# Kernel tuning notes

Hardware: AMD Instinct MI355X
Metric: run time of the kernel (lower is better)

Reference implementation:

```python
import jax, jax.numpy as jnp
import numpy as np

BITS_W = 2  # WAGE default weight bitwidth


def _scale(bits):
    return 2.0 ** (bits - 1)


def quantize_w(x):
    """WAGE Quantize.W: clip to [-1+delta, 1-delta], round to grid of step delta,
    with straight-through estimator for gradients."""
    s = _scale(BITS_W)
    delta = 1.0 / s
    xc = jnp.clip(x, -1.0 + delta, 1.0 - delta)
    y = jnp.round(xc * s) / s
    # straight-through: forward uses y, gradient flows as identity to x
    return x + jax.lax.stop_gradient(y - x)


def setup_inputs() -> dict:
    key = jax.random.key(0)
    k1, k2 = jax.random.split(key)
    B, D_IN, C_OUT = 16384, 1024, 1024
    inputs = jax.random.normal(k1, (B, D_IN), dtype=jnp.float32)
    # learned kernel per build(): shape [d_in, c_out]
    kernel = jax.random.normal(k2, (D_IN, C_OUT), dtype=jnp.float32) * 0.5
    return {"inputs": inputs, "kernel": kernel}


def reference(inputs, kernel):
    # quantize weights every forward pass, then dense matmul
    return jnp.matmul(inputs, quantize_w(kernel))
```

## Files before the change

kernel.cpp:

```cpp
#include <hip/hip_runtime.h>

typedef unsigned short u16;
typedef unsigned int u32;

typedef __bf16 bf16x8 __attribute__((ext_vector_type(8)));
typedef float floatx4 __attribute__((ext_vector_type(4)));


__device__ __forceinline__ u32 f2bf(float f) {
    u32 u = __builtin_bit_cast(u32, f);
    return (u + 0x7fffu + ((u >> 16) & 1u)) >> 16;
}

__device__ __forceinline__ float quant_w(float x) {
    float xc = fminf(fmaxf(x, -0.5f), 0.5f);
    return rintf(xc * 2.0f) * 0.5f;
}

__device__ __forceinline__ void gload_lds16(const u16* g, u16* l) {
    __builtin_amdgcn_global_load_lds(
        (const __attribute__((address_space(1))) void*)g,
        (__attribute__((address_space(3))) void*)l,
        16, 0, 0);
}


__global__ __launch_bounds__(256) void cast_a_kernel(const float4* __restrict__ in,
                                                     uint4* __restrict__ out) {
    int t = blockIdx.x * 256 + threadIdx.x;
    float4 a = in[2 * t];
    float4 b = in[2 * t + 1];
    uint4 o;
    o.x = f2bf(a.x) | (f2bf(a.y) << 16);
    o.y = f2bf(a.z) | (f2bf(a.w) << 16);
    o.z = f2bf(b.x) | (f2bf(b.y) << 16);
    o.w = f2bf(b.z) | (f2bf(b.w) << 16);
    out[t] = o;
}


__global__ __launch_bounds__(256) void quant_transpose_kernel(const float* __restrict__ W,
                                                              u16* __restrict__ Bt) {
    __shared__ u16 tile[32][33];
    const int KN = 1024;
    int tx = threadIdx.x;
    int ty = threadIdx.y;
    int k0 = blockIdx.y * 32;
    int n0 = blockIdx.x * 32;
#pragma unroll
    for (int i = 0; i < 4; i++) {
        int kl = ty + i * 8;
        float x = W[(k0 + kl) * KN + n0 + tx];
        tile[kl][tx] = (u16)f2bf(quant_w(x));
    }
    __syncthreads();
#pragma unroll
    for (int i = 0; i < 4; i++) {
        int nl = ty + i * 8;
        Bt[(n0 + nl) * KN + k0 + tx] = tile[tx][nl];
    }
}


__global__ __launch_bounds__(512, 2) void gemm_4region_kernel(const u16* __restrict__ A,
                                                              const u16* __restrict__ Bt,
                                                              float* __restrict__ C) {
    const int K = 1024;
    const int N = 1024;

    __shared__ alignas(16) u16 As[2 * 2 * 128 * 64];
    __shared__ alignas(16) u16 Bs[2 * 2 * 128 * 64];

    const int tid = threadIdx.x;
    const int lane = tid & 63;
    const int wid = tid >> 6;
    const int wm = wid >> 2;
    const int wn = wid & 3;
    const int frow = lane & 15;
    const int fkc = lane >> 4;
    const int rsw = frow & 7;
    const int mbase = blockIdx.x * 256;
    const int nbase = blockIdx.y * 256;

    const int sr = tid >> 3;
    const int gc = (tid & 7) ^ (sr & 7);

    const u16* Abase = &A[(size_t)(mbase + sr) * K + gc * 8];
    const u16* Bbase = &Bt[(size_t)(nbase + sr) * K + gc * 8];

    floatx4 acc[8][4] = {};
    bf16x8 af0[4][2], af1[4][2], bf0[2][2], bf1[2][2];

    auto stage = [&](int tau, int q) {
        const int hf = q & 1;
        const int isA = q >> 1;
        const u16* gb = isA ? Abase : Bbase;
        u16* lb = isA ? As : Bs;
        const size_t goff = (size_t)(hf * 128) * K + (size_t)tau * 64;
        u16* dst = &lb[(((tau & 1) * 2 + hf) * 8192) + tid * 8];
        gload_lds16(gb + goff, dst);
        gload_lds16(gb + goff + (size_t)64 * K, dst + 4096);
    };

#define LGKM0() asm volatile("s_waitcnt lgkmcnt(0)" ::: "memory")
#define VMC(n)  asm volatile("s_waitcnt vmcnt(" #n ")" ::: "memory")
#define BAR()                          \
    __builtin_amdgcn_sched_barrier(0); \
    __builtin_amdgcn_s_barrier();      \
    __builtin_amdgcn_sched_barrier(0)

#define READ_AF0(b)                                                                  \
    _Pragma("unroll") for (int mf = 0; mf < 4; mf++)                                 \
        _Pragma("unroll") for (int s = 0; s < 2; s++)                                \
            af0[mf][s] = *(const bf16x8*)&As[(((b)*2 + wm) * 128 + mf * 16 + frow) * 64 + \
                                             (((s * 4 + fkc) ^ rsw) * 8)]
#define READ_AF1(b)                                                                  \
    _Pragma("unroll") for (int mf = 0; mf < 4; mf++)                                 \
        _Pragma("unroll") for (int s = 0; s < 2; s++)                                \
            af1[mf][s] = *(const bf16x8*)&As[(((b)*2 + wm) * 128 + 64 + mf * 16 + frow) * 64 + \
                                             (((s * 4 + fkc) ^ rsw) * 8)]
#define READ_BF0(b)                                                                  \
    _Pragma("unroll") for (int nf = 0; nf < 2; nf++)                                 \
        _Pragma("unroll") for (int s = 0; s < 2; s++)                                \
            bf0[nf][s] = *(const bf16x8*)&Bs[(((b)*2 + (wn >> 1)) * 128 + (wn & 1) * 64 + nf * 16 + frow) * 64 + \
                                             (((s * 4 + fkc) ^ rsw) * 8)]
#define READ_BF1(b)                                                                  \
    _Pragma("unroll") for (int nf = 0; nf < 2; nf++)                                 \
        _Pragma("unroll") for (int s = 0; s < 2; s++)                                \
            bf1[nf][s] = *(const bf16x8*)&Bs[(((b)*2 + (wn >> 1)) * 128 + (wn & 1) * 64 + 32 + nf * 16 + frow) * 64 + \
                                             (((s * 4 + fkc) ^ rsw) * 8)]
#define MFMA_CL(af, bf, mo, no)                                                      \
    __builtin_amdgcn_s_setprio(1);                                                   \
    _Pragma("unroll") for (int mf = 0; mf < 4; mf++)                                 \
        _Pragma("unroll") for (int nf = 0; nf < 2; nf++)                             \
            _Pragma("unroll") for (int s = 0; s < 2; s++)                            \
                acc[(mo) + mf][(no) + nf] = __builtin_amdgcn_mfma_f32_16x16x32_bf16( \
                    af[mf][s], bf[nf][s], acc[(mo) + mf][(no) + nf], 0, 0, 0);       \
    __builtin_amdgcn_s_setprio(0)

    stage(0, 0); stage(0, 1); stage(0, 2); stage(0, 3);
    stage(1, 0); stage(1, 1); stage(1, 2); stage(1, 3);
    VMC(8);
    BAR();

    for (int t = 0; t < 16; t++) {
        const int b = t & 1;

        if (t > 0) { MFMA_CL(af1, bf1, 4, 2); }
        READ_AF0(b);
        READ_BF0(b);
        LGKM0();
        BAR();

        MFMA_CL(af0, bf0, 0, 0);
        READ_AF1(b);
        LGKM0();
        BAR();

        MFMA_CL(af1, bf0, 4, 0);
        READ_BF1(b);
        if (t <= 13) { stage(t + 2, 2); stage(t + 2, 3); }
        LGKM0();
        BAR();

        MFMA_CL(af0, bf1, 0, 2);
        if (t <= 13) {
            stage(t + 2, 0); stage(t + 2, 1);
            VMC(8);
        } else if (t == 14) {
            VMC(0);
        }
        BAR();
    }

    MFMA_CL(af1, bf1, 4, 2);

#undef LGKM0
#undef VMC
#undef BAR
#undef READ_AF0
#undef READ_AF1
#undef READ_BF0
#undef READ_BF1
#undef MFMA_CL

    const int crow = (lane >> 4) * 4;
    const int ccol = lane & 15;
#pragma unroll
    for (int i = 0; i < 8; i++) {
#pragma unroll
        for (int j = 0; j < 4; j++) {
            float* cp = &C[(size_t)(mbase + wm * 128 + i * 16 + crow) * N +
                           nbase + wn * 64 + j * 16 + ccol];
#pragma unroll
            for (int r = 0; r < 4; r++) cp[r * N] = acc[i][j][r];
        }
    }
}


extern "C" void kernel_launch(void* const* d_in, const int* in_sizes, int n_in,
                              void* d_out, int out_size, void* d_ws, size_t ws_size,
                              hipStream_t stream) {
    const float* A = (const float*)d_in[0];
    const float* W = (const float*)d_in[1];
    float* C = (float*)d_out;

    u16* Abf = (u16*)d_ws;
    u16* Btq = (u16*)((char*)d_ws + (size_t)33554432);

    cast_a_kernel<<<8192, 256, 0, stream>>>((const float4*)A, (uint4*)Abf);
    quant_transpose_kernel<<<dim3(32, 32), dim3(32, 8), 0, stream>>>(W, Btq);
    gemm_4region_kernel<<<dim3(64, 4), 512, 0, stream>>>(Abf, Btq, C);
}
```

Before: 145.2 us.

## Restructure GEMM main loop into two barrier regions with split-row staging

The GEMM main loop drops from four barrier-separated regions per K-step to two. Each tile's global-to-LDS loads are split into two row halves: one half is issued two steps ahead and the other one step ahead, with matching vmcnt waits. All A and B fragment reads are now issued together before three back-to-back MFMA clusters, cutting barrier count and sync stalls at the cost of more live registers and tighter load/compute overlap. The cast kernel also has each thread convert two chunks, halving its grid size.

```diff
diff --git a/kernel.cpp b/kernel.cpp
--- a/kernel.cpp
+++ b/kernel.cpp
@@ -28,14 +28,17 @@
 __global__ __launch_bounds__(256) void cast_a_kernel(const float4* __restrict__ in,
                                                      uint4* __restrict__ out) {
     int t = blockIdx.x * 256 + threadIdx.x;
-    float4 a = in[2 * t];
-    float4 b = in[2 * t + 1];
-    uint4 o;
-    o.x = f2bf(a.x) | (f2bf(a.y) << 16);
-    o.y = f2bf(a.z) | (f2bf(a.w) << 16);
-    o.z = f2bf(b.x) | (f2bf(b.y) << 16);
-    o.w = f2bf(b.z) | (f2bf(b.w) << 16);
-    out[t] = o;
+#pragma unroll
+    for (int u = 0; u < 2; u++) {
+        float4 a = in[4 * t + 2 * u];
+        float4 b = in[4 * t + 2 * u + 1];
+        uint4 o;
+        o.x = f2bf(a.x) | (f2bf(a.y) << 16);
+        o.y = f2bf(a.z) | (f2bf(a.w) << 16);
+        o.z = f2bf(b.x) | (f2bf(b.y) << 16);
+        o.w = f2bf(b.z) | (f2bf(b.w) << 16);
+        out[2 * t + u] = o;
+    }
 }
 
 
@@ -62,7 +65,7 @@
 }
 
 
-__global__ __launch_bounds__(512, 2) void gemm_4region_kernel(const u16* __restrict__ A,
+__global__ __launch_bounds__(512, 2) void gemm_2region_kernel(const u16* __restrict__ A,
                                                               const u16* __restrict__ Bt,
                                                               float* __restrict__ C) {
     const int K = 1024;
@@ -84,22 +87,28 @@
 
     const int sr = tid >> 3;
     const int gc = (tid & 7) ^ (sr & 7);
-
-    const u16* Abase = &A[(size_t)(mbase + sr) * K + gc * 8];
-    const u16* Bbase = &Bt[(size_t)(nbase + sr) * K + gc * 8];
+    const int brow0 = ((sr >> 5) << 6) | (sr & 31);
 
     floatx4 acc[8][4] = {};
     bf16x8 af0[4][2], af1[4][2], bf0[2][2], bf1[2][2];
 
-    auto stage = [&](int tau, int q) {
-        const int hf = q & 1;
-        const int isA = q >> 1;
-        const u16* gb = isA ? Abase : Bbase;
-        u16* lb = isA ? As : Bs;
-        const size_t goff = (size_t)(hf * 128) * K + (size_t)tau * 64;
-        u16* dst = &lb[(((tau & 1) * 2 + hf) * 8192) + tid * 8];
-        gload_lds16(gb + goff, dst);
-        gload_lds16(gb + goff + (size_t)64 * K, dst + 4096);
+    auto astage = [&](int tau, int u) {
+        const int row = sr + u * 64;
+#pragma unroll
+        for (int hf = 0; hf < 2; hf++) {
+            const u16* g = &A[(size_t)(mbase + hf * 128 + row) * K + (size_t)tau * 64 + gc * 8];
+            u16* dst = &As[(((tau & 1) * 2 + hf) * 8192) + row * 64 + (tid & 7) * 8];
+            gload_lds16(g, dst);
+        }
+    };
+    auto bstage = [&](int tau, int u) {
+        const int row = brow0 + u * 32;
+#pragma unroll
+        for (int hf = 0; hf < 2; hf++) {
+            const u16* g = &Bt[(size_t)(nbase + hf * 128 + row) * K + (size_t)tau * 64 + gc * 8];
+            u16* dst = &Bs[(((tau & 1) * 2 + hf) * 8192) + row * 64 + (tid & 7) * 8];
+            gload_lds16(g, dst);
+        }
     };
 
 #define LGKM0() asm volatile("s_waitcnt lgkmcnt(0)" ::: "memory")
@@ -138,8 +147,9 @@
                     af[mf][s], bf[nf][s], acc[(mo) + mf][(no) + nf], 0, 0, 0);       \
     __builtin_amdgcn_s_setprio(0)
 
-    stage(0, 0); stage(0, 1); stage(0, 2); stage(0, 3);
-    stage(1, 0); stage(1, 1); stage(1, 2); stage(1, 3);
+    astage(0, 0); bstage(0, 0);
+    astage(0, 1); bstage(0, 1);
+    astage(1, 0); bstage(1, 0);
     VMC(8);
     BAR();
 
@@ -149,27 +159,27 @@
         if (t > 0) { MFMA_CL(af1, bf1, 4, 2); }
         READ_AF0(b);
         READ_BF0(b);
+        if (t <= 14) {
+            astage(t + 1, 1); bstage(t + 1, 1);
+            VMC(8);
+        } else {
+            VMC(0);
+        }
         LGKM0();
         BAR();
 
+        READ_AF1(b);
+        READ_BF1(b);
         MFMA_CL(af0, bf0, 0, 0);
-        READ_AF1(b);
-        LGKM0();
-        BAR();
-
         MFMA_CL(af1, bf0, 4, 0);
-        READ_BF1(b);
-        if (t <= 13) { stage(t + 2, 2); stage(t + 2, 3); }
-        LGKM0();
-        BAR();
-
         MFMA_CL(af0, bf1, 0, 2);
         if (t <= 13) {
-            stage(t + 2, 0); stage(t + 2, 1);
+            astage(t + 2, 0); bstage(t + 2, 0);
             VMC(8);
         } else if (t == 14) {
-            VMC(0);
-        }
+            VMC(4);
+        }
+        LGKM0();
         BAR();
     }
 
@@ -209,7 +219,7 @@
     u16* Abf = (u16*)d_ws;
     u16* Btq = (u16*)((char*)d_ws + (size_t)33554432);
 
-    cast_a_kernel<<<8192, 256, 0, stream>>>((const float4*)A, (uint4*)Abf);
+    cast_a_kernel<<<4096, 256, 0, stream>>>((const float4*)A, (uint4*)Abf);
     quant_transpose_kernel<<<dim3(32, 32), dim3(32, 8), 0, stream>>>(W, Btq);
-    gemm_4region_kernel<<<dim3(64, 4), 512, 0, stream>>>(Abf, Btq, C);
-}
+    gemm_2region_kernel<<<dim3(64, 4), 512, 0, stream>>>(Abf, Btq, C);
+}
```

Result: no change. 147.2 us (+1.4%).
